# Optimization experiments

Measured on AMD Instinct MI355X. Metric: run time of the kernel, lower is better.

The kernel has to match this reference:

```python
import jax, jax.numpy as jnp
import numpy as np

B, N, M, K = 8, 9225, 4096, 32
D = 2          # coordinate dim
HID = 64       # MLP hidden
DOUT = 16      # MLP output / f_y channels


def setup_inputs() -> dict:
    key = jax.random.key(0)
    ks = jax.random.split(key, 10)
    y = jax.random.uniform(ks[0], (B, N, D), dtype=jnp.float32)
    x = jax.random.uniform(ks[1], (B, M, D), dtype=jnp.float32)
    f_y = jax.random.uniform(ks[2], (B, N, DOUT), dtype=jnp.float32)
    weights = jax.random.uniform(ks[3], (B, N), dtype=jnp.float32)
    neighbors_index = jax.random.randint(ks[4], (B, M, K), 0, N, dtype=jnp.int64)
    drop = jax.random.uniform(ks[5], (B, M, K)) < 0.1
    neighbors_index = jnp.where(drop, jnp.int64(-1), neighbors_index)
    # LinearChannelMLP params: 4 -> 64 -> 16, gelu between
    W1 = jax.random.normal(ks[6], (2 * D, HID), dtype=jnp.float32) * (1.0 / np.sqrt(2 * D))
    b1 = jnp.zeros((HID,), dtype=jnp.float32)
    W2 = jax.random.normal(ks[7], (HID, DOUT), dtype=jnp.float32) * (1.0 / np.sqrt(HID))
    b2 = jnp.zeros((DOUT,), dtype=jnp.float32)
    return {"y": y, "x": x, "f_y": f_y, "weights": weights,
            "W1": W1, "b1": b1, "W2": W2, "b2": b2,
            "neighbors_index": neighbors_index}


def _batched_gather(table, idx):
    # table: [B, N, ...], idx: [B, M, K] -> [B, M, K, ...]
    return jax.vmap(lambda t, i: t[i])(table, idx)


def reference(y, x, f_y, weights, W1, b1, W2, b2, neighbors_index):
    idx = jnp.where(neighbors_index == -1, 0, neighbors_index)      # [B,M,K]
    valid = (neighbors_index != -1).astype(y.dtype)[..., None]      # [B,M,K,1]

    rep_y = _batched_gather(y, idx)                                 # [B,M,K,D]
    in_f = _batched_gather(f_y, idx)                                # [B,M,K,DOUT]
    self_x = jnp.broadcast_to(x[:, :, None, :], rep_y.shape)        # [B,M,K,D]

    agg = jnp.concatenate([rep_y, self_x], axis=-1)                 # [B,M,K,2D]
    h = jax.nn.gelu(agg @ W1 + b1, approximate=False)               # [B,M,K,HID]
    kval = h @ W2 + b2                                              # [B,M,K,DOUT]

    kval = kval * in_f                                              # linear transform: k(x,y)*f(y)
    w_nbr = _batched_gather(weights, idx)[..., None]                # [B,M,K,1]
    kval = kval * w_nbr * valid
    return kval.sum(axis=2)                                         # [B,M,DOUT]
```

## Files before the change

### kernel.cpp

```cpp
#include <hip/hip_runtime.h>
#include <hip/hip_bf16.h>

#define B_    8
#define N_    9225
#define M_    4096
#define K_    32
#define HID_  64
#define DOUT_ 16

typedef __attribute__((ext_vector_type(8))) short short8;
typedef __attribute__((ext_vector_type(4))) float floatx4;
typedef __attribute__((ext_vector_type(2))) float f32x2;

static __device__ __forceinline__ short f2bf(float f) {
    __hip_bfloat16 h = __float2bfloat16(f);
    return __builtin_bit_cast(short, h);
}
static __device__ __forceinline__ f32x2 splat2(float v) { return (f32x2){v, v}; }
static __device__ __forceinline__ int bpermi(int src_bytes, int v) {
    return __builtin_amdgcn_ds_bpermute(src_bytes, v);
}
static __device__ __forceinline__ float bpermf(int src_bytes, float v) {
    return __builtin_bit_cast(float,
        __builtin_amdgcn_ds_bpermute(src_bytes, __builtin_bit_cast(int, v)));
}

static __device__ __forceinline__ float row16_sum(float v) {
    int t;
    t = __builtin_amdgcn_update_dpp(0, __builtin_bit_cast(int, v), 0x111, 0xF, 0xF, true);
    v += __builtin_bit_cast(float, t);
    t = __builtin_amdgcn_update_dpp(0, __builtin_bit_cast(int, v), 0x112, 0xF, 0xF, true);
    v += __builtin_bit_cast(float, t);
    t = __builtin_amdgcn_update_dpp(0, __builtin_bit_cast(int, v), 0x114, 0xF, 0xF, true);
    v += __builtin_bit_cast(float, t);
    t = __builtin_amdgcn_update_dpp(0, __builtin_bit_cast(int, v), 0x118, 0xF, 0xF, true);
    v += __builtin_bit_cast(float, t);
    return v;
}

static __device__ __forceinline__ f32x2 gelu2(f32x2 x) {
    const f32x2 xsq = x * x;
    const f32x2 t   = __builtin_elementwise_fma(xsq, splat2(0.035677408f), splat2(0.79788456f));
    const f32x2 z   = x * t;
    const f32x2 u   = z * z;
    const f32x2 a   = u + splat2(105.0f);
    const f32x2 nin = __builtin_elementwise_fma(u, a, splat2(945.0f));
    const f32x2 num = z * nin;
    const f32x2 bq  = __builtin_elementwise_fma(u, splat2(15.0f), splat2(420.0f));
    const f32x2 den = __builtin_elementwise_fma(u, bq, splat2(945.0f));
    const f32x2 r   = { __builtin_amdgcn_rcpf(den[0]), __builtin_amdgcn_rcpf(den[1]) };
    f32x2 th = num * r;
    th = __builtin_elementwise_min(__builtin_elementwise_max(th, splat2(-1.0f)), splat2(1.0f));
    const f32x2 hx = x * splat2(0.5f);
    return __builtin_elementwise_fma(hx, th, hx);
}

__global__ __launch_bounds__(256) void it_kernel(
    const float* __restrict__ y,
    const float* __restrict__ x,
    const float* __restrict__ f_y,
    const float* __restrict__ weights,
    const float* __restrict__ W1,
    const float* __restrict__ b1,
    const float* __restrict__ W2,
    const float* __restrict__ b2,
    const int*   __restrict__ nbr,
    float*       __restrict__ out)
{
    __shared__ float W1L[4][64];
    __shared__ float b1L[64];
    __shared__ float b2L[16];

    const int tid  = threadIdx.x;
    W1L[tid >> 6][tid & 63] = W1[tid];
    if (tid < 64) b1L[tid] = b1[tid];
    if (tid < 16) b2L[tid] = b2[tid];

    const int lane = tid & 63;
    const int q    = lane >> 4;
    const int nlo  = lane & 15;
    const int blk   = blockIdx.x;
    const int batch = blk & 7;
    const int pidx  = (blk >> 3) * 4 + (tid >> 6);
    const int row0  = __builtin_amdgcn_readfirstlane(batch * M_ + pidx * 2);
    const int bbase = batch * N_;

    const int r_g = lane >> 5, kk = lane & 31;
    const int raw = nbr[(size_t)(row0 + r_g) * K_ + kk];
    const int vld = raw >= 0;
    const int bn_g = bbase + (vld ? raw : 0);
    const float2 yvg = *(const float2*)(y + (size_t)bn_g * 2);
    const float  wg  = vld ? weights[bn_g] : 0.0f;

    short8 w2f[2];
    #pragma unroll
    for (int ch = 0; ch < 2; ++ch)
        #pragma unroll
        for (int jj = 0; jj < 8; ++jj)
            w2f[ch][jj] = f2bf(W2[(ch*32 + q*8 + jj) * DOUT_ + nlo]);

    __syncthreads();

    float partial[4] = {0.f, 0.f, 0.f, 0.f};
    #pragma unroll
    for (int ph = 0; ph < 4; ++ph) {
        const int it = ph >> 1, h = ph & 1;
        const int src = ((it << 5) + (h << 4) + nlo) << 2;

        const int bn = bpermi(src, bn_g);
        const floatx4 fv = *(const floatx4*)(f_y + (size_t)bn * 16 + q * 4);

        f32x2 yv;
        yv[0] = bpermf(src, yvg.x);
        yv[1] = bpermf(src, yvg.y);
        const float s = bpermf(src, wg);
        const float2 xv = *(const float2*)(x + (size_t)(row0 + it) * 2);

        short8 hf[2];
        #pragma unroll
        for (int ch = 0; ch < 2; ++ch) {
            #pragma unroll
            for (int p = 0; p < 4; ++p) {
                const int j = ch*32 + q*8 + 2*p;
                f32x2 hin = *(const f32x2*)&b1L[j];
                hin = __builtin_elementwise_fma(splat2(yv[0]), *(const f32x2*)&W1L[0][j], hin);
                hin = __builtin_elementwise_fma(splat2(yv[1]), *(const f32x2*)&W1L[1][j], hin);
                hin = __builtin_elementwise_fma(splat2(xv.x),  *(const f32x2*)&W1L[2][j], hin);
                hin = __builtin_elementwise_fma(splat2(xv.y),  *(const f32x2*)&W1L[3][j], hin);
                const f32x2 g = gelu2(hin);
                hf[ch][2*p]     = f2bf(g[0]);
                hf[ch][2*p + 1] = f2bf(g[1]);
            }
        }
        floatx4 acc = *(const floatx4*)&b2L[q*4];
        acc = __builtin_amdgcn_mfma_f32_16x16x32_bf16(w2f[0], hf[0], acc, 0, 0, 0);
        acc = __builtin_amdgcn_mfma_f32_16x16x32_bf16(w2f[1], hf[1], acc, 0, 0, 0);
        #pragma unroll
        for (int r4 = 0; r4 < 4; ++r4)
            partial[r4] = fmaf(acc[r4], fv[r4] * s, partial[r4]);

        if (h == 1) {
            #pragma unroll
            for (int r4 = 0; r4 < 4; ++r4)
                partial[r4] = row16_sum(partial[r4]);
            if (nlo == 15) {
                floatx4 o = {partial[0], partial[1], partial[2], partial[3]};
                *(floatx4*)(out + (size_t)(row0 + it) * DOUT_ + q*4) = o;
            }
            #pragma unroll
            for (int r4 = 0; r4 < 4; ++r4) partial[r4] = 0.f;
        }
    }
}

extern "C" void kernel_launch(void* const* d_in, const int* in_sizes, int n_in,
                              void* d_out, int out_size, void* d_ws, size_t ws_size,
                              hipStream_t stream) {
    const float* y   = (const float*)d_in[0];
    const float* x   = (const float*)d_in[1];
    const float* f_y = (const float*)d_in[2];
    const float* w   = (const float*)d_in[3];
    const float* W1  = (const float*)d_in[4];
    const float* b1  = (const float*)d_in[5];
    const float* W2  = (const float*)d_in[6];
    const float* b2  = (const float*)d_in[7];
    const int*   nbr = (const int*)d_in[8];
    float* out = (float*)d_out;

    dim3 grid(B_ * M_ / 8), block(256);
    hipLaunchKernelGGL(it_kernel, grid, block, 0, stream,
                       y, x, f_y, w, W1, b1, W2, b2, nbr, out);
}
```

Baseline: 105.2 us.

## Compute first MLP layer with split-bf16 MFMA and prefetch gathers across rows

Replaces the per-lane scalar FMA first layer (4->64) with MFMA instructions, using a hi/lo bf16 split of the inputs to keep accuracy, and permutes the W2 layout so MFMA outputs feed the second MFMA directly. Each wave now handles 4 rows instead of 2, with neighbor gathers software-pipelined two phases ahead. Cross-lane bpermute shuffles are removed, and launch bounds request 4 blocks per CU. The cost is more registers for the prefetch buffers and extra MFMAs that are mostly zero-padded.

```diff
diff --git a/kernel.cpp b/kernel.cpp
--- a/kernel.cpp
+++ b/kernel.cpp
@@ -16,14 +16,11 @@
     __hip_bfloat16 h = __float2bfloat16(f);
     return __builtin_bit_cast(short, h);
 }
+static __device__ __forceinline__ float bf2f(short s) {
+    unsigned u = ((unsigned)(unsigned short)s) << 16;
+    return __builtin_bit_cast(float, u);
+}
 static __device__ __forceinline__ f32x2 splat2(float v) { return (f32x2){v, v}; }
-static __device__ __forceinline__ int bpermi(int src_bytes, int v) {
-    return __builtin_amdgcn_ds_bpermute(src_bytes, v);
-}
-static __device__ __forceinline__ float bpermf(int src_bytes, float v) {
-    return __builtin_bit_cast(float,
-        __builtin_amdgcn_ds_bpermute(src_bytes, __builtin_bit_cast(int, v)));
-}
 
 static __device__ __forceinline__ float row16_sum(float v) {
     int t;
@@ -55,7 +52,7 @@
     return __builtin_elementwise_fma(hx, th, hx);
 }
 
-__global__ __launch_bounds__(256) void it_kernel(
+__global__ __launch_bounds__(256, 4) void it_kernel(
     const float* __restrict__ y,
     const float* __restrict__ x,
     const float* __restrict__ f_y,
@@ -67,90 +64,135 @@
     const int*   __restrict__ nbr,
     float*       __restrict__ out)
 {
-    __shared__ float W1L[4][64];
     __shared__ float b1L[64];
     __shared__ float b2L[16];
 
-    const int tid  = threadIdx.x;
-    W1L[tid >> 6][tid & 63] = W1[tid];
+    const int tid = threadIdx.x;
     if (tid < 64) b1L[tid] = b1[tid];
     if (tid < 16) b2L[tid] = b2[tid];
 
     const int lane = tid & 63;
     const int q    = lane >> 4;
     const int nlo  = lane & 15;
+
     const int blk   = blockIdx.x;
     const int batch = blk & 7;
-    const int pidx  = (blk >> 3) * 4 + (tid >> 6);
-    const int row0  = __builtin_amdgcn_readfirstlane(batch * M_ + pidx * 2);
+    const int pblk  = blk >> 3;
+    const int wid   = tid >> 6;
+    const int row0  = __builtin_amdgcn_readfirstlane(batch * M_ + pblk * 16 + wid * 4);
     const int bbase = batch * N_;
 
-    const int r_g = lane >> 5, kk = lane & 31;
-    const int raw = nbr[(size_t)(row0 + r_g) * K_ + kk];
-    const int vld = raw >= 0;
-    const int bn_g = bbase + (vld ? raw : 0);
-    const float2 yvg = *(const float2*)(y + (size_t)bn_g * 2);
-    const float  wg  = vld ? weights[bn_g] : 0.0f;
+    short8 w1h[4];
+    #pragma unroll
+    for (int t = 0; t < 4; ++t) {
+        #pragma unroll
+        for (int jj = 0; jj < 8; ++jj) w1h[t][jj] = 0;
+        #pragma unroll
+        for (int jj = 0; jj < 4; ++jj) {
+            const float wv = W1[jj * HID_ + t * 16 + nlo];
+            w1h[t][jj] = (q == 0) ? f2bf(wv) : (short)0;
+        }
+    }
 
     short8 w2f[2];
     #pragma unroll
     for (int ch = 0; ch < 2; ++ch)
         #pragma unroll
-        for (int jj = 0; jj < 8; ++jj)
-            w2f[ch][jj] = f2bf(W2[(ch*32 + q*8 + jj) * DOUT_ + nlo]);
+        for (int jj = 0; jj < 8; ++jj) {
+            const int H = (ch * 2 + (jj >> 2)) * 16 + q * 4 + (jj & 3);
+            w2f[ch][jj] = f2bf(W2[H * DOUT_ + nlo]);
+        }
+
+    short xh[8], xl[8];
+    #pragma unroll
+    for (int it = 0; it < 4; ++it) {
+        const float2 xv = *(const float2*)(x + (size_t)(row0 + it) * 2);
+        const short h0 = f2bf(xv.x); const short l0 = f2bf(xv.x - bf2f(h0));
+        const short h1 = f2bf(xv.y); const short l1 = f2bf(xv.y - bf2f(h1));
+        xh[it * 2] = h0; xh[it * 2 + 1] = h1;
+        xl[it * 2] = l0; xl[it * 2 + 1] = l1;
+    }
+
+    int raw[8];
+    #pragma unroll
+    for (int ph = 0; ph < 8; ++ph) {
+        const int it = ph >> 1, h = ph & 1;
+        raw[ph] = nbr[(size_t)(row0 + it) * K_ + h * 16 + nlo];
+    }
+
+    float2 yv[8]; float sw[8]; floatx4 fv[8];
+    #define GATH(P) { \
+        const int rv  = raw[P]; \
+        const int vld = rv >= 0; \
+        const int bn  = bbase + (vld ? rv : 0); \
+        yv[P] = *(const float2*)(y + (size_t)bn * 2); \
+        const float wv_ = weights[bn]; \
+        sw[P] = vld ? wv_ : 0.0f; \
+        fv[P] = *(const floatx4*)(f_y + (size_t)bn * DOUT_ + q * 4); \
+    }
+    GATH(0); GATH(1);
 
     __syncthreads();
 
     float partial[4] = {0.f, 0.f, 0.f, 0.f};
     #pragma unroll
-    for (int ph = 0; ph < 4; ++ph) {
-        const int it = ph >> 1, h = ph & 1;
-        const int src = ((it << 5) + (h << 4) + nlo) << 2;
-
-        const int bn = bpermi(src, bn_g);
-        const floatx4 fv = *(const floatx4*)(f_y + (size_t)bn * 16 + q * 4);
-
-        f32x2 yv;
-        yv[0] = bpermf(src, yvg.x);
-        yv[1] = bpermf(src, yvg.y);
-        const float s = bpermf(src, wg);
-        const float2 xv = *(const float2*)(x + (size_t)(row0 + it) * 2);
-
-        short8 hf[2];
-        #pragma unroll
-        for (int ch = 0; ch < 2; ++ch) {
+    for (int ph = 0; ph < 8; ++ph) {
+        if (ph + 2 < 8) GATH(ph + 2);
+        const int it = ph >> 1;
+
+        const float y0 = yv[ph].x, y1 = yv[ph].y;
+        const short yh0 = f2bf(y0); const short yl0 = f2bf(y0 - bf2f(yh0));
+        const short yh1 = f2bf(y1); const short yl1 = f2bf(y1 - bf2f(yh1));
+        const bool q0 = (q == 0);
+        const short z = 0;
+        const short8 bhi = { q0 ? yh0 : z, q0 ? yh1 : z,
+                             q0 ? xh[it * 2] : z, q0 ? xh[it * 2 + 1] : z,
+                             z, z, z, z };
+        const short8 blo = { q0 ? yl0 : z, q0 ? yl1 : z,
+                             q0 ? xl[it * 2] : z, q0 ? xl[it * 2 + 1] : z,
+                             z, z, z, z };
+
+        floatx4 a1[4];
+        #pragma unroll
+        for (int t = 0; t < 4; ++t) {
+            a1[t] = *(const floatx4*)&b1L[t * 16 + q * 4];
+            a1[t] = __builtin_amdgcn_mfma_f32_16x16x32_bf16(w1h[t], bhi, a1[t], 0, 0, 0);
+            a1[t] = __builtin_amdgcn_mfma_f32_16x16x32_bf16(w1h[t], blo, a1[t], 0, 0, 0);
+        }
+
+        short hv[16];
+        #pragma unroll
+        for (int t = 0; t < 4; ++t) {
+            const f32x2 g01 = gelu2((f32x2){a1[t][0], a1[t][1]});
+            const f32x2 g23 = gelu2((f32x2){a1[t][2], a1[t][3]});
+            hv[t * 4 + 0] = f2bf(g01[0]); hv[t * 4 + 1] = f2bf(g01[1]);
+            hv[t * 4 + 2] = f2bf(g23[0]); hv[t * 4 + 3] = f2bf(g23[1]);
+        }
+        const short8 hf0 = {hv[0], hv[1], hv[2],  hv[3],  hv[4],  hv[5],  hv[6],  hv[7]};
+        const short8 hf1 = {hv[8], hv[9], hv[10], hv[11], hv[12], hv[13], hv[14], hv[15]};
+
+        floatx4 acc = *(const floatx4*)&b2L[q * 4];
+        acc = __builtin_amdgcn_mfma_f32_16x16x32_bf16(w2f[0], hf0, acc, 0, 0, 0);
+        acc = __builtin_amdgcn_mfma_f32_16x16x32_bf16(w2f[1], hf1, acc, 0, 0, 0);
+
+        const floatx4 fvp = fv[ph];
+        const float   s   = sw[ph];
+        #pragma unroll
+        for (int r = 0; r < 4; ++r)
+            partial[r] = fmaf(acc[r], fvp[r] * s, partial[r]);
+
+        if (ph & 1) {
             #pragma unroll
-            for (int p = 0; p < 4; ++p) {
-                const int j = ch*32 + q*8 + 2*p;
-                f32x2 hin = *(const f32x2*)&b1L[j];
-                hin = __builtin_elementwise_fma(splat2(yv[0]), *(const f32x2*)&W1L[0][j], hin);
-                hin = __builtin_elementwise_fma(splat2(yv[1]), *(const f32x2*)&W1L[1][j], hin);
-                hin = __builtin_elementwise_fma(splat2(xv.x),  *(const f32x2*)&W1L[2][j], hin);
-                hin = __builtin_elementwise_fma(splat2(xv.y),  *(const f32x2*)&W1L[3][j], hin);
-                const f32x2 g = gelu2(hin);
-                hf[ch][2*p]     = f2bf(g[0]);
-                hf[ch][2*p + 1] = f2bf(g[1]);
-            }
-        }
-        floatx4 acc = *(const floatx4*)&b2L[q*4];
-        acc = __builtin_amdgcn_mfma_f32_16x16x32_bf16(w2f[0], hf[0], acc, 0, 0, 0);
-        acc = __builtin_amdgcn_mfma_f32_16x16x32_bf16(w2f[1], hf[1], acc, 0, 0, 0);
-        #pragma unroll
-        for (int r4 = 0; r4 < 4; ++r4)
-            partial[r4] = fmaf(acc[r4], fv[r4] * s, partial[r4]);
-
-        if (h == 1) {
-            #pragma unroll
-            for (int r4 = 0; r4 < 4; ++r4)
-                partial[r4] = row16_sum(partial[r4]);
+            for (int r = 0; r < 4; ++r) partial[r] = row16_sum(partial[r]);
             if (nlo == 15) {
                 floatx4 o = {partial[0], partial[1], partial[2], partial[3]};
-                *(floatx4*)(out + (size_t)(row0 + it) * DOUT_ + q*4) = o;
+                *(floatx4*)(out + (size_t)(row0 + it) * DOUT_ + q * 4) = o;
             }
             #pragma unroll
-            for (int r4 = 0; r4 < 4; ++r4) partial[r4] = 0.f;
-        }
-    }
+            for (int r = 0; r < 4; ++r) partial[r] = 0.f;
+        }
+    }
+    #undef GATH
 }
 
 extern "C" void kernel_launch(void* const* d_in, const int* in_sizes, int n_in,
@@ -167,7 +209,7 @@
     const int*   nbr = (const int*)d_in[8];
     float* out = (float*)d_out;
 
-    dim3 grid(B_ * M_ / 8), block(256);
+    dim3 grid(B_ * M_ / 16), block(256);
     hipLaunchKernelGGL(it_kernel, grid, block, 0, stream,
                        y, x, f_y, w, W1, b1, W2, b2, nbr, out);
 }
```

Result: slower. 108.7 us (+3.3%).
